# Optimization experiments

Hardware: AMD Instinct MI355X
Metric: run time of the kernel (lower is better)

## Reference

```python
import jax, jax.numpy as jnp
import numpy as np
import math

EPS = 1e-12


def _cmul(ar, ai, br, bi):
    return ar * br - ai * bi, ar * bi + ai * br


def _wilson_seed(x):
    # x: (B, 4, L, L) -> conj of canonical Wilson-line path, (B, L, L) re/im
    ux_r, ux_i, uy_r, uy_i = x[:, 0], x[:, 1], x[:, 2], x[:, 3]
    B, L, _ = ux_r.shape
    dt = x.dtype

    def step(c, u):
        cr, ci = c
        ur, ui = u
        nr, ni = _cmul(cr, ci, ur, ui)
        return (nr, ni), (nr, ni)

    # cumulative complex product along x at y=0
    init_r = jnp.ones((B,), dt)
    init_i = jnp.zeros((B,), dt)
    xs = (ux_r[:, :-1, 0].T, ux_i[:, :-1, 0].T)  # (L-1, B)
    _, (axr, axi) = jax.lax.scan(step, (init_r, init_i), xs)
    x_axis_r = jnp.concatenate([init_r[None], axr], 0).T  # (B, L)
    x_axis_i = jnp.concatenate([init_i[None], axi], 0).T

    # cumulative complex product along y, vectorized over x
    ys = (jnp.moveaxis(uy_r[:, :, :-1], 2, 0), jnp.moveaxis(uy_i[:, :, :-1], 2, 0))  # (L-1, B, L)
    _, (pr, pi_) = jax.lax.scan(step, (x_axis_r, x_axis_i), ys)
    path_r = jnp.moveaxis(jnp.concatenate([x_axis_r[None], pr], 0), 0, 2)  # (B, L, L)
    path_i = jnp.moveaxis(jnp.concatenate([x_axis_i[None], pi_], 0), 0, 2)
    return path_r, -path_i  # conjugate


def _wrap(t):
    return (t + math.pi) % (2.0 * math.pi) - math.pi


def _initial_features(x):
    seed_r, seed_i = _wilson_seed(x)
    ax = jnp.arctan2(x[:, 1], x[:, 0])
    ay = jnp.arctan2(x[:, 3], x[:, 2])
    plaq = _wrap(ax + jnp.roll(ay, -1, axis=1) - jnp.roll(ax, -1, axis=2) - ay)
    pc = jnp.cos(plaq)
    pavg = (pc + jnp.roll(pc, 1, 1) + jnp.roll(pc, -1, 1)
            + jnp.roll(pc, 1, 2) + jnp.roll(pc, -1, 2)) / 5.0
    scalars = jnp.stack([jnp.ones_like(pc), pc, pavg], axis=1)  # (B, 3, L, L)
    return seed_r[:, None] * scalars, seed_i[:, None] * scalars


def _transport_fwd(fr, fi, x, mu):
    lr, li = (x[:, 0], x[:, 1]) if mu == 0 else (x[:, 2], x[:, 3])
    sr = jnp.roll(fr, -1, axis=mu + 2)
    si = jnp.roll(fi, -1, axis=mu + 2)
    return _cmul(lr[:, None], li[:, None], sr, si)


def _transport_bwd(fr, fi, x, mu):
    lr, li = (x[:, 0], x[:, 1]) if mu == 0 else (x[:, 2], x[:, 3])
    cr = jnp.roll(lr, 1, axis=mu + 1)
    ci = jnp.roll(-li, 1, axis=mu + 1)
    sr = jnp.roll(fr, 1, axis=mu + 2)
    si = jnp.roll(fi, 1, axis=mu + 2)
    return _cmul(cr[:, None], ci[:, None], sr, si)


def _lconv(fr, fi, x, center, fwd_w, bwd_w):
    out_r = jnp.einsum('oi,bixy->boxy', center, fr)
    out_i = jnp.einsum('oi,bixy->boxy', center, fi)
    for mu in range(2):
        fr2, fi2 = _transport_fwd(fr, fi, x, mu)
        br2, bi2 = _transport_bwd(fr, fi, x, mu)
        out_r = out_r + jnp.einsum('oi,bixy->boxy', fwd_w[mu], fr2) \
                      + jnp.einsum('oi,bixy->boxy', bwd_w[mu], br2)
        out_i = out_i + jnp.einsum('oi,bixy->boxy', fwd_w[mu], fi2) \
                      + jnp.einsum('oi,bixy->boxy', bwd_w[mu], bi2)
    return out_r, out_i


def _modrelu(fr, fi, bias):
    mag = jnp.sqrt(fr * fr + fi * fi + EPS)
    act = jax.nn.relu(mag + bias[None, :, None, None])
    scale = act / jnp.maximum(mag, EPS)
    return fr * scale, fi * scale


def setup_inputs() -> dict:
    key = jax.random.key(0)
    ks = jax.random.split(key, 11)
    B, L, H, O = 64, 128, 16, 8
    s = 0.1
    return {
        'x': jax.random.normal(ks[0], (B, 4, L, L), jnp.float32),
        'center1': s * jax.random.normal(ks[1], (H, 3), jnp.float32),
        'fwd_w1': s * jax.random.normal(ks[2], (2, H, 3), jnp.float32),
        'bwd_w1': s * jax.random.normal(ks[3], (2, H, 3), jnp.float32),
        'bias1': jnp.zeros((H,), jnp.float32),
        'center2': s * jax.random.normal(ks[4], (O, H), jnp.float32),
        'fwd_w2': s * jax.random.normal(ks[5], (2, O, H), jnp.float32),
        'bwd_w2': s * jax.random.normal(ks[6], (2, O, H), jnp.float32),
        'bias2': jnp.zeros((O,), jnp.float32),
        'ro_weight': s * jax.random.normal(ks[7], (O,), jnp.float32),
        'ro_bias': jnp.zeros((1,), jnp.float32),
    }


def reference(x, center1, fwd_w1, bwd_w1, bias1, center2, fwd_w2, bwd_w2, bias2, ro_weight, ro_bias):
    fr, fi = _initial_features(x)
    fr, fi = _lconv(fr, fi, x, center1, fwd_w1, bwd_w1)
    fr, fi = _modrelu(fr, fi, bias1)
    fr, fi = _lconv(fr, fi, x, center2, fwd_w2, bwd_w2)
    fr, fi = _modrelu(fr, fi, bias2)
    inv = fr * fr + fi * fi
    return jnp.einsum('c,bcxy->bxy', ro_weight, inv)[:, None] + ro_bias.reshape(1, 1, 1, 1)
```

## Files before the change

kernel.cpp:

```cpp
#include <hip/hip_runtime.h>
#include <math.h>

#define LQ   128
#define BQ   64
#define LL   (LQ*LQ)
#define H1   16
#define O2   8
#define TILE 16
#define REG  18
#define NPTS (REG*REG)
#define PCR  22
#define PCN  (PCR*PCR)
#define LKR  23
#define LKN  (LKR*LKR)
#define SDR  20
#define SDN  (SDR*SDR)
#define FSTR 10

typedef float f2 __attribute__((ext_vector_type(2)));
using bf8 = __attribute__((ext_vector_type(8))) short;
using f4  = __attribute__((ext_vector_type(4))) float;

__device__ __forceinline__ int wrapi(int v) { return v & (LQ - 1); }

__device__ __forceinline__ unsigned pack_bf(float hi, float lo) {
    return __builtin_amdgcn_perm(__float_as_uint(hi), __float_as_uint(lo),
                                 0x07060302u);
}

#define WS_W1 ((size_t)BQ * LL)

__global__ __launch_bounds__(256)
void k_scan(const float* __restrict__ x,
            const float* __restrict__ c1, const float* __restrict__ fw1,
            const float* __restrict__ bw1, float* __restrict__ ws) {
    int blk = blockIdx.x;
    if (blk == BQ * 8) {
        int tid = threadIdx.x;
        if (tid < 120) {
            int t = tid / 24, r = tid - t * 24;
            int c = r >> 3, op = r & 7;
            const float* src = (t == 0) ? c1 : (t == 1) ? fw1 : (t == 2) ? bw1
                             : (t == 3) ? (fw1 + 48) : (bw1 + 48);
            float2 v = make_float2(src[(2 * op) * 3 + c], src[(2 * op + 1) * 3 + c]);
            ((float2*)ws)[WS_W1 + tid] = v;
        }
        return;
    }
    int b = blk >> 3, rq = blk & 7;
    int l = threadIdx.x & 63, w = threadIdx.x >> 6;
    const float* x0 = x + (size_t)b * 4 * LL;
    const float* x1 = x0 + LL;

    float ur0 = x0[(2 * l) * LQ],     ui0 = x1[(2 * l) * LQ];
    float ur1 = x0[(2 * l + 1) * LQ], ui1 = x1[(2 * l + 1) * LQ];
    float pr = ur0 * ur1 - ui0 * ui1;
    float pi = ur0 * ui1 + ui0 * ur1;
    for (int d = 1; d < 64; d <<= 1) {
        float qr = __shfl_up(pr, d, 64);
        float qi = __shfl_up(pi, d, 64);
        if (l >= d) {
            float nr = qr * pr - qi * pi;
            float ni = qr * pi + qi * pr;
            pr = nr; pi = ni;
        }
    }
    float er = __shfl_up(pr, 1, 64);
    float ei = __shfl_up(pi, 1, 64);
    if (l == 0) { er = 1.f; ei = 0.f; }
    float e1r = er * ur0 - ei * ui0;
    float e1i = er * ui0 + ei * ur0;

    const float* yrp = x + (size_t)(b * 4 + 2) * LL;
    const float* yip = yrp + LL;
    float4* seed4 = (float4*)ws;

    for (int k = 0; k < 4; ++k) {
        int i = rq * 16 + w * 4 + k;
        float cxr = __shfl((i & 1) ? e1r : er, i >> 1, 64);
        float cxi = __shfl((i & 1) ? e1i : ei, i >> 1, 64);
        const float* yr = yrp + (size_t)i * LQ;
        const float* yi = yip + (size_t)i * LQ;
        float vr0 = yr[2 * l],     vi0 = yi[2 * l];
        float vr1 = yr[2 * l + 1], vi1 = yi[2 * l + 1];
        float sr = vr0 * vr1 - vi0 * vi1;
        float si = vr0 * vi1 + vi0 * vr1;
        for (int d = 1; d < 64; d <<= 1) {
            float qr = __shfl_up(sr, d, 64);
            float qi = __shfl_up(si, d, 64);
            if (l >= d) {
                float nr = qr * sr - qi * si;
                float ni = qr * si + qi * sr;
                sr = nr; si = ni;
            }
        }
        float gr = __shfl_up(sr, 1, 64);
        float gi = __shfl_up(si, 1, 64);
        if (l == 0) { gr = 1.f; gi = 0.f; }
        float s0r = cxr * gr - cxi * gi;
        float s0i = cxr * gi + cxi * gr;
        float s1r = s0r * vr0 - s0i * vi0;
        float s1i = s0r * vi0 + s0i * vr0;
        seed4[((size_t)b * LL + (size_t)i * LQ) / 2 + l] =
            make_float4(s0r, -s0i, s1r, -s1i);
    }
}

__global__ __launch_bounds__(256, 4)
void k_main(const float* __restrict__ x,
            const float* __restrict__ c2, const float* __restrict__ fw2,
            const float* __restrict__ bw2, const float* __restrict__ b1,
            const float* __restrict__ b2,
            const float* __restrict__ ro, const float* __restrict__ rob,
            const float* __restrict__ ws, float* __restrict__ out) {
    __shared__ unsigned s_f1r[NPTS * FSTR];
    __shared__ unsigned s_f1i[NPTS * FSTR];
    __shared__ f2 s_ux[LKN];
    __shared__ f2 s_uy[LKN];
    __shared__ float s_pc[PCN];
    __shared__ f2 s_sd[SDN];
    int tid = threadIdx.x;
    int b = blockIdx.z, i0 = blockIdx.y * TILE, j0 = blockIdx.x * TILE;
    const float* x0 = x + (size_t)b * 4 * LL;
    const float* x1 = x0 + LL;
    const float* x2 = x0 + 2 * LL;
    const float* x3 = x0 + 3 * LL;
    const float2* seed = (const float2*)ws + (size_t)b * LL;
    const float2* W1 = (const float2*)ws + WS_W1;

    bool z1 = true;
#pragma unroll
    for (int h = 0; h < H1; ++h) z1 = z1 && (b1[h] == 0.f);
    bool z2 = true;
#pragma unroll
    for (int o = 0; o < O2; ++o) z2 = z2 && (b2[o] == 0.f);

    for (int p = tid; p < LKN; p += 256) {
        int ri = p / LKR, rj = p - ri * LKR;
        int gi = wrapi(i0 - 3 + ri), gj = wrapi(j0 - 3 + rj);
        int idx = gi * LQ + gj;
        s_ux[p] = (f2){x0[idx], x1[idx]};
        s_uy[p] = (f2){x2[idx], x3[idx]};
    }
    for (int p = tid; p < SDN; p += 256) {
        int ri = p / SDR, rj = p - ri * SDR;
        int gi = wrapi(i0 - 2 + ri), gj = wrapi(j0 - 2 + rj);
        float2 s = seed[gi * LQ + gj];
        s_sd[p] = (f2){s.x, s.y};
    }
    __syncthreads();

    for (int p = tid; p < PCN; p += 256) {
        int ri = p / PCR, rj = p - ri * PCR;
        int lb = ri * LKR + rj;
        f2 u1 = s_ux[lb];
        f2 u2 = s_uy[lb + LKR];
        f2 u3 = s_ux[lb + 1];
        f2 u4 = s_uy[lb];
        float ar = u1.x * u2.x - u1.y * u2.y, ai = u1.x * u2.y + u1.y * u2.x;
        float br = ar * u3.x + ai * u3.y,     bi = -ar * u3.y + ai * u3.x;
        float zr = br * u4.x + bi * u4.y,     zi = -br * u4.y + bi * u4.x;
        s_pc[p] = zr * __frsqrt_rn(fmaf(zr, zr, zi * zi) + 1e-30f);
    }
    __syncthreads();

#pragma unroll
    for (int pass = 0; pass < 2; ++pass) {
        int p = tid + pass * 256;
        if (pass == 1 && p >= NPTS) break;
        int ri = p / REG, rj = p - ri * REG;
        int sc = (ri + 1) * SDR + (rj + 1);
        int lb = (ri + 2) * LKR + (rj + 2);
        int cb = (ri + 2) * PCR + (rj + 2);

        f2 t[5]; float tc[5], tv[5];
        {
            f2 SC = s_sd[sc], SXP = s_sd[sc + SDR], SXM = s_sd[sc - SDR];
            f2 SYP = s_sd[sc + 1], SYM = s_sd[sc - 1];
            f2 lx = s_ux[lb], ly = s_uy[lb];
            f2 mx = s_ux[lb - LKR], my = s_uy[lb - 1];
            t[0] = SC;
            t[1] = (f2){lx.x * SXP.x - lx.y * SXP.y, lx.x * SXP.y + lx.y * SXP.x};
            t[2] = (f2){mx.x * SXM.x + mx.y * SXM.y, mx.x * SXM.y - mx.y * SXM.x};
            t[3] = (f2){ly.x * SYP.x - ly.y * SYP.y, ly.x * SYP.y + ly.y * SYP.x};
            t[4] = (f2){my.x * SYM.x + my.y * SYM.y, my.x * SYM.y - my.y * SYM.x};
            float p00 = s_pc[cb];
            float pP0 = s_pc[cb + PCR],     pM0 = s_pc[cb - PCR];
            float p0P = s_pc[cb + 1],       p0M = s_pc[cb - 1];
            float pP20 = s_pc[cb + 2*PCR],  pM20 = s_pc[cb - 2*PCR];
            float p0P2 = s_pc[cb + 2],      p0M2 = s_pc[cb - 2];
            float pPP = s_pc[cb + PCR + 1], pPM = s_pc[cb + PCR - 1];
            float pMP = s_pc[cb - PCR + 1], pMM = s_pc[cb - PCR - 1];
            tc[0] = p00; tc[1] = pP0; tc[2] = pM0; tc[3] = p0P; tc[4] = p0M;
            tv[0] = (p00 + pP0 + pM0 + p0P + p0M) * 0.2f;
            tv[1] = (pP0 + pP20 + p00 + pPP + pPM) * 0.2f;
            tv[2] = (pM0 + p00 + pM20 + pMP + pMM) * 0.2f;
            tv[3] = (p0P + pPP + pMP + p0P2 + p00) * 0.2f;
            tv[4] = (p0M + pPM + pMM + p00 + p0M2) * 0.2f;
        }

        f2 accr[8], acci[8];
#pragma unroll
        for (int op = 0; op < 8; ++op) { accr[op] = (f2){0.f, 0.f}; acci[op] = (f2){0.f, 0.f}; }
#pragma unroll
        for (int q = 0; q < 5; ++q) {
            f2 tcv = (f2){tc[q], tc[q]}, tvv = (f2){tv[q], tv[q]};
            f2 trv = (f2){t[q].x, t[q].x}, tiv = (f2){t[q].y, t[q].y};
            const float2* Wq = W1 + q * 24;
#pragma unroll
            for (int op = 0; op < 8; ++op) {
                float2 w0 = Wq[op], w1 = Wq[8 + op], w2 = Wq[16 + op];
                f2 mp = (f2){w0.x, w0.y};
                mp += (f2){w1.x, w1.y} * tcv;
                mp += (f2){w2.x, w2.y} * tvv;
                accr[op] += mp * trv;
                acci[op] += mp * tiv;
            }
        }
        if (!z1) {
#pragma unroll
            for (int op = 0; op < 8; ++op) {
                f2 q2 = accr[op] * accr[op] + acci[op] * acci[op] + (f2){1e-12f, 1e-12f};
                float s0 = fmaxf(fmaf(b1[2 * op],     __frsqrt_rn(q2.x), 1.f), 0.f);
                float s1 = fmaxf(fmaf(b1[2 * op + 1], __frsqrt_rn(q2.y), 1.f), 0.f);
                f2 sv = (f2){s0, s1};
                accr[op] *= sv; acci[op] *= sv;
            }
        }
        unsigned* fr_ = &s_f1r[p * FSTR];
        unsigned* fi_ = &s_f1i[p * FSTR];
#pragma unroll
        for (int d = 0; d < 4; ++d) {
            unsigned r0 = pack_bf(accr[2*d].y,   accr[2*d].x);
            unsigned r1 = pack_bf(accr[2*d+1].y, accr[2*d+1].x);
            unsigned q0 = pack_bf(acci[2*d].y,   acci[2*d].x);
            unsigned q1 = pack_bf(acci[2*d+1].y, acci[2*d+1].x);
            *(uint2*)&fr_[2*d] = make_uint2(r0, r1);
            *(uint2*)&fi_[2*d] = make_uint2(q0, q1);
        }
    }
    __syncthreads();

    int lane = tid & 63, w = tid >> 6;
    int quad = lane >> 4, nIdx = lane & 15;
    int half = quad >> 1;
    int koff = (quad & 1) * 4;

    const float* wLo[3] = {c2, bw2, bw2 + O2 * H1};
    const float* wHi[3] = {fw2, fw2 + O2 * H1, (const float*)0};
    bf8 afr[3];
#pragma unroll
    for (int pq = 0; pq < 3; ++pq) {
        bf8 z = {0, 0, 0, 0, 0, 0, 0, 0};
        const float* wsrc = half ? wHi[pq] : wLo[pq];
        int row = half ? (nIdx - 8) : nIdx;
        bool valid = half ? (nIdx >= 8 && wsrc != 0) : (nIdx < 8);
        if (valid) {
            const float* wp = wsrc + row * H1 + (quad & 1) * 8;
            float4 wa = *(const float4*)wp;
            float4 wb = *(const float4*)(wp + 4);
            uint4 u;
            u.x = pack_bf(wa.y, wa.x);
            u.y = pack_bf(wa.w, wa.z);
            u.z = pack_bf(wb.y, wb.x);
            u.w = pack_bf(wb.w, wb.z);
            __builtin_memcpy(&z, &u, 16);
        }
        afr[pq] = z;
    }
    float4 ro_lo = *(const float4*)ro;
    float4 ro_hi = *(const float4*)(ro + 4);
    float4 b2_lo = *(const float4*)b2;
    float4 b2_hi = *(const float4*)(b2 + 4);
    float4 zf4 = make_float4(0.f, 0.f, 0.f, 0.f);
    float4 rv = (quad == 0) ? ro_lo : ((quad == 1) ? ro_hi : zf4);
    float4 bv = (quad == 0) ? b2_lo : ((quad == 1) ? b2_hi : zf4);
    float rob0 = rob[0];

    for (int g = 0; g < 4; ++g) {
        int row = w * 4 + g;
        int posc = (row + 1) * REG + (nIdx + 1);
        int lb2 = (row + 3) * LKR + (nIdx + 3);
        f2 lx = s_ux[lb2], ly = s_uy[lb2];
        f2 mx = s_ux[lb2 - LKR], my = s_uy[lb2 - 1];

        float Lr[3], Li[3];
        Lr[0] = half ? lx.x : 1.f;   Li[0] = half ? lx.y : 0.f;
        Lr[1] = half ? ly.x : mx.x;  Li[1] = half ? ly.y : -mx.y;
        Lr[2] = half ? 0.f : my.x;   Li[2] = half ? 0.f : -my.y;
        int dpl[3];
        dpl[0] = half ? REG : 0;
        dpl[1] = half ? 1 : -REG;
        dpl[2] = -1;

        f4 a2r = {0.f, 0.f, 0.f, 0.f}, a2i = {0.f, 0.f, 0.f, 0.f};
#pragma unroll
        for (int pq = 0; pq < 3; ++pq) {
            int base = (posc + dpl[pq]) * FSTR + koff;
            uint2 rlo = *(const uint2*)&s_f1r[base];
            uint2 rhi = *(const uint2*)&s_f1r[base + 2];
            uint2 ilo = *(const uint2*)&s_f1i[base];
            uint2 ihi = *(const uint2*)&s_f1i[base + 2];
            bf8 br, bi;
            uint4 ur = {rlo.x, rlo.y, rhi.x, rhi.y};
            uint4 ui = {ilo.x, ilo.y, ihi.x, ihi.y};
            __builtin_memcpy(&br, &ur, 16);
            __builtin_memcpy(&bi, &ui, 16);
            f4 zc = {0.f, 0.f, 0.f, 0.f};
            f4 sr = __builtin_amdgcn_mfma_f32_16x16x32_bf16(afr[pq], br, zc, 0, 0, 0);
            f4 si = __builtin_amdgcn_mfma_f32_16x16x32_bf16(afr[pq], bi, zc, 0, 0, 0);
            a2r += Lr[pq] * sr - Li[pq] * si;
            a2i += Lr[pq] * si + Li[pq] * sr;
        }

#pragma unroll
        for (int c = 0; c < 4; ++c) {
            a2r[c] += __shfl_xor(a2r[c], 32, 64);
            a2i[c] += __shfl_xor(a2i[c], 32, 64);
        }

        f4 q4 = a2r * a2r + a2i * a2i;
        float res;
        if (z2) {
            res = rv.x * q4.x + rv.y * q4.y + rv.z * q4.z + rv.w * q4.w;
        } else {
            float bvv[4] = {bv.x, bv.y, bv.z, bv.w};
            float rvv[4] = {rv.x, rv.y, rv.z, rv.w};
            res = 0.f;
#pragma unroll
            for (int r = 0; r < 4; ++r) {
                float qq = q4[r];
                float s = fmaxf(fmaf(bvv[r], __frsqrt_rn(qq + 1e-12f), 1.f), 0.f);
                res = fmaf(rvv[r], s * s * qq, res);
            }
        }
        res += __shfl_xor(res, 16, 64);
        if (quad == 0)
            out[(size_t)b * LL + (size_t)(i0 + row) * LQ + (j0 + nIdx)] = res + rob0;
    }
}

extern "C" void kernel_launch(void* const* d_in, const int* in_sizes, int n_in,
                              void* d_out, int out_size, void* d_ws, size_t ws_size,
                              hipStream_t stream) {
    const float* x   = (const float*)d_in[0];
    const float* c1  = (const float*)d_in[1];
    const float* fw1 = (const float*)d_in[2];
    const float* bw1 = (const float*)d_in[3];
    const float* b1  = (const float*)d_in[4];
    const float* c2  = (const float*)d_in[5];
    const float* fw2 = (const float*)d_in[6];
    const float* bw2 = (const float*)d_in[7];
    const float* b2  = (const float*)d_in[8];
    const float* ro  = (const float*)d_in[9];
    const float* rob = (const float*)d_in[10];
    float* out = (float*)d_out;
    float* ws  = (float*)d_ws;

    k_scan<<<BQ * 8 + 1, 256, 0, stream>>>(x, c1, fw1, bw1, ws);
    dim3 grid(LQ / TILE, LQ / TILE, BQ);
    k_main<<<grid, 256, 0, stream>>>(x, c2, fw2, bw2, b1, b2,
                                     ro, rob, ws, out);
}
```

Baseline: 135.3 us.

## Compute first lattice conv layer with bf16 MFMA and swizzled shared layout

Layer 1 of the lattice convolution was scalar FMA over 5 transports x 3 scalars x 16 channels. It now builds a 15-wide bf16 feature vector per point, transposes it across lanes with shuffles, and multiplies by the layer-1 weight matrix with 16x16x32 bf16 MFMA. The seed staging buffer in shared memory is dropped in favour of direct global reads. Layer-1 output moves to a single rotated/swizzled 16-word-per-point LDS layout so layer 2 can use 128-bit loads, and occupancy is raised to 5 blocks per CU. Costs include extra shuffles and lower precision in layer 1, since inputs are rounded to bf16 before the multiply.

```diff
diff --git a/kernel.cpp b/kernel.cpp
--- a/kernel.cpp
+++ b/kernel.cpp
@@ -13,9 +13,6 @@
 #define PCN  (PCR*PCR)
 #define LKR  23
 #define LKN  (LKR*LKR)
-#define SDR  20
-#define SDN  (SDR*SDR)
-#define FSTR 10
 
 typedef float f2 __attribute__((ext_vector_type(2)));
 using bf8 = __attribute__((ext_vector_type(8))) short;
@@ -26,6 +23,11 @@
 __device__ __forceinline__ unsigned pack_bf(float hi, float lo) {
     return __builtin_amdgcn_perm(__float_as_uint(hi), __float_as_uint(lo),
                                  0x07060302u);
+}
+__device__ __forceinline__ unsigned cvt_pk_bf16(float lo, float hi) {
+    unsigned r;
+    asm("v_cvt_pk_bf16_f32 %0, %1, %2" : "=v"(r) : "v"(lo), "v"(hi));
+    return r;
 }
 
 #define WS_W1 ((size_t)BQ * LL)
@@ -106,19 +108,17 @@
     }
 }
 
-__global__ __launch_bounds__(256, 4)
+__global__ __launch_bounds__(256, 5)
 void k_main(const float* __restrict__ x,
             const float* __restrict__ c2, const float* __restrict__ fw2,
             const float* __restrict__ bw2, const float* __restrict__ b1,
             const float* __restrict__ b2,
             const float* __restrict__ ro, const float* __restrict__ rob,
             const float* __restrict__ ws, float* __restrict__ out) {
-    __shared__ unsigned s_f1r[NPTS * FSTR];
-    __shared__ unsigned s_f1i[NPTS * FSTR];
+    __shared__ __align__(16) unsigned s_f1[NPTS * 16];
     __shared__ f2 s_ux[LKN];
     __shared__ f2 s_uy[LKN];
     __shared__ float s_pc[PCN];
-    __shared__ f2 s_sd[SDN];
     int tid = threadIdx.x;
     int b = blockIdx.z, i0 = blockIdx.y * TILE, j0 = blockIdx.x * TILE;
     const float* x0 = x + (size_t)b * 4 * LL;
@@ -128,12 +128,34 @@
     const float2* seed = (const float2*)ws + (size_t)b * LL;
     const float2* W1 = (const float2*)ws + WS_W1;
 
+    int lane = tid & 63, w = tid >> 6;
+    int kc = lane >> 4, h = lane & 15, half = kc >> 1;
+
     bool z1 = true;
 #pragma unroll
-    for (int h = 0; h < H1; ++h) z1 = z1 && (b1[h] == 0.f);
+    for (int hh = 0; hh < H1; ++hh) z1 = z1 && (b1[hh] == 0.f);
     bool z2 = true;
 #pragma unroll
-    for (int o = 0; o < O2; ++o) z2 = z2 && (b2[o] == 0.f);
+    for (int oo = 0; oo < O2; ++oo) z2 = z2 && (b2[oo] == 0.f);
+
+    bf8 a1 = {0, 0, 0, 0, 0, 0, 0, 0};
+    if (kc < 2) {
+        float v[8];
+#pragma unroll
+        for (int j = 0; j < 8; ++j) {
+            int k = kc * 8 + j;
+            float val = 0.f;
+            if (k < 15) {
+                int q = k / 3, c = k - q * 3;
+                val = ((const float*)(W1 + (q * 24 + c * 8 + (h >> 1))))[h & 1];
+            }
+            v[j] = val;
+        }
+        unsigned dw[4];
+#pragma unroll
+        for (int d = 0; d < 4; ++d) dw[d] = cvt_pk_bf16(v[2 * d], v[2 * d + 1]);
+        __builtin_memcpy(&a1, dw, 16);
+    }
 
     for (int p = tid; p < LKN; p += 256) {
         int ri = p / LKR, rj = p - ri * LKR;
@@ -141,12 +163,6 @@
         int idx = gi * LQ + gj;
         s_ux[p] = (f2){x0[idx], x1[idx]};
         s_uy[p] = (f2){x2[idx], x3[idx]};
-    }
-    for (int p = tid; p < SDN; p += 256) {
-        int ri = p / SDR, rj = p - ri * SDR;
-        int gi = wrapi(i0 - 2 + ri), gj = wrapi(j0 - 2 + rj);
-        float2 s = seed[gi * LQ + gj];
-        s_sd[p] = (f2){s.x, s.y};
     }
     __syncthreads();
 
@@ -164,87 +180,105 @@
     }
     __syncthreads();
 
-#pragma unroll
-    for (int pass = 0; pass < 2; ++pass) {
-        int p = tid + pass * 256;
-        if (pass == 1 && p >= NPTS) break;
-        int ri = p / REG, rj = p - ri * REG;
-        int sc = (ri + 1) * SDR + (rj + 1);
+    for (int wp = w * 64; wp < NPTS; wp += 256) {
+        int p = wp + lane;
+        int pp = (p < NPTS) ? p : (NPTS - 1);
+        int ri = pp / REG, rj = pp - ri * REG;
         int lb = (ri + 2) * LKR + (rj + 2);
         int cb = (ri + 2) * PCR + (rj + 2);
 
-        f2 t[5]; float tc[5], tv[5];
+        int gi0 = wrapi(i0 - 1 + ri), gim = wrapi(i0 - 2 + ri), gip = wrapi(i0 + ri);
+        int gj0 = wrapi(j0 - 1 + rj), gjm = wrapi(j0 - 2 + rj), gjp = wrapi(j0 + rj);
+        float2 SC  = seed[gi0 * LQ + gj0];
+        float2 SXP = seed[gip * LQ + gj0];
+        float2 SXM = seed[gim * LQ + gj0];
+        float2 SYP = seed[gi0 * LQ + gjp];
+        float2 SYM = seed[gi0 * LQ + gjm];
+
+        f2 lx = s_ux[lb], ly = s_uy[lb];
+        f2 mx = s_ux[lb - LKR], my = s_uy[lb - 1];
+        float tr[5], ti[5], tc[5], tv[5];
+        tr[0] = SC.x;                          ti[0] = SC.y;
+        tr[1] = lx.x * SXP.x - lx.y * SXP.y;   ti[1] = lx.x * SXP.y + lx.y * SXP.x;
+        tr[2] = mx.x * SXM.x + mx.y * SXM.y;   ti[2] = mx.x * SXM.y - mx.y * SXM.x;
+        tr[3] = ly.x * SYP.x - ly.y * SYP.y;   ti[3] = ly.x * SYP.y + ly.y * SYP.x;
+        tr[4] = my.x * SYM.x + my.y * SYM.y;   ti[4] = my.x * SYM.y - my.y * SYM.x;
+
+        float p00 = s_pc[cb];
+        float pP0 = s_pc[cb + PCR],     pM0 = s_pc[cb - PCR];
+        float p0P = s_pc[cb + 1],       p0M = s_pc[cb - 1];
+        float pP20 = s_pc[cb + 2*PCR],  pM20 = s_pc[cb - 2*PCR];
+        float p0P2 = s_pc[cb + 2],      p0M2 = s_pc[cb - 2];
+        float pPP = s_pc[cb + PCR + 1], pPM = s_pc[cb + PCR - 1];
+        float pMP = s_pc[cb - PCR + 1], pMM = s_pc[cb - PCR - 1];
+        tc[0] = p00; tc[1] = pP0; tc[2] = pM0; tc[3] = p0P; tc[4] = p0M;
+        tv[0] = (p00 + pP0 + pM0 + p0P + p0M) * 0.2f;
+        tv[1] = (pP0 + pP20 + p00 + pPP + pPM) * 0.2f;
+        tv[2] = (pM0 + p00 + pM20 + pMP + pMM) * 0.2f;
+        tv[3] = (p0P + pPP + pMP + p0P2 + p00) * 0.2f;
+        tv[4] = (p0M + pPM + pMM + p00 + p0M2) * 0.2f;
+
+        unsigned fr8[8], fi8[8];
         {
-            f2 SC = s_sd[sc], SXP = s_sd[sc + SDR], SXM = s_sd[sc - SDR];
-            f2 SYP = s_sd[sc + 1], SYM = s_sd[sc - 1];
-            f2 lx = s_ux[lb], ly = s_uy[lb];
-            f2 mx = s_ux[lb - LKR], my = s_uy[lb - 1];
-            t[0] = SC;
-            t[1] = (f2){lx.x * SXP.x - lx.y * SXP.y, lx.x * SXP.y + lx.y * SXP.x};
-            t[2] = (f2){mx.x * SXM.x + mx.y * SXM.y, mx.x * SXM.y - mx.y * SXM.x};
-            t[3] = (f2){ly.x * SYP.x - ly.y * SYP.y, ly.x * SYP.y + ly.y * SYP.x};
-            t[4] = (f2){my.x * SYM.x + my.y * SYM.y, my.x * SYM.y - my.y * SYM.x};
-            float p00 = s_pc[cb];
-            float pP0 = s_pc[cb + PCR],     pM0 = s_pc[cb - PCR];
-            float p0P = s_pc[cb + 1],       p0M = s_pc[cb - 1];
-            float pP20 = s_pc[cb + 2*PCR],  pM20 = s_pc[cb - 2*PCR];
-            float p0P2 = s_pc[cb + 2],      p0M2 = s_pc[cb - 2];
-            float pPP = s_pc[cb + PCR + 1], pPM = s_pc[cb + PCR - 1];
-            float pMP = s_pc[cb - PCR + 1], pMM = s_pc[cb - PCR - 1];
-            tc[0] = p00; tc[1] = pP0; tc[2] = pM0; tc[3] = p0P; tc[4] = p0M;
-            tv[0] = (p00 + pP0 + pM0 + p0P + p0M) * 0.2f;
-            tv[1] = (pP0 + pP20 + p00 + pPP + pPM) * 0.2f;
-            tv[2] = (pM0 + p00 + pM20 + pMP + pMM) * 0.2f;
-            tv[3] = (p0P + pPP + pMP + p0P2 + p00) * 0.2f;
-            tv[4] = (p0M + pPM + pMM + p00 + p0M2) * 0.2f;
-        }
-
-        f2 accr[8], acci[8];
-#pragma unroll
-        for (int op = 0; op < 8; ++op) { accr[op] = (f2){0.f, 0.f}; acci[op] = (f2){0.f, 0.f}; }
-#pragma unroll
-        for (int q = 0; q < 5; ++q) {
-            f2 tcv = (f2){tc[q], tc[q]}, tvv = (f2){tv[q], tv[q]};
-            f2 trv = (f2){t[q].x, t[q].x}, tiv = (f2){t[q].y, t[q].y};
-            const float2* Wq = W1 + q * 24;
-#pragma unroll
-            for (int op = 0; op < 8; ++op) {
-                float2 w0 = Wq[op], w1 = Wq[8 + op], w2 = Wq[16 + op];
-                f2 mp = (f2){w0.x, w0.y};
-                mp += (f2){w1.x, w1.y} * tcv;
-                mp += (f2){w2.x, w2.y} * tvv;
-                accr[op] += mp * trv;
-                acci[op] += mp * tiv;
-            }
-        }
-        if (!z1) {
-#pragma unroll
-            for (int op = 0; op < 8; ++op) {
-                f2 q2 = accr[op] * accr[op] + acci[op] * acci[op] + (f2){1e-12f, 1e-12f};
-                float s0 = fmaxf(fmaf(b1[2 * op],     __frsqrt_rn(q2.x), 1.f), 0.f);
-                float s1 = fmaxf(fmaf(b1[2 * op + 1], __frsqrt_rn(q2.y), 1.f), 0.f);
-                f2 sv = (f2){s0, s1};
-                accr[op] *= sv; acci[op] *= sv;
-            }
-        }
-        unsigned* fr_ = &s_f1r[p * FSTR];
-        unsigned* fi_ = &s_f1i[p * FSTR];
-#pragma unroll
-        for (int d = 0; d < 4; ++d) {
-            unsigned r0 = pack_bf(accr[2*d].y,   accr[2*d].x);
-            unsigned r1 = pack_bf(accr[2*d+1].y, accr[2*d+1].x);
-            unsigned q0 = pack_bf(acci[2*d].y,   acci[2*d].x);
-            unsigned q1 = pack_bf(acci[2*d+1].y, acci[2*d+1].x);
-            *(uint2*)&fr_[2*d] = make_uint2(r0, r1);
-            *(uint2*)&fi_[2*d] = make_uint2(q0, q1);
+            float Fr[16], Fi[16];
+#pragma unroll
+            for (int q = 0; q < 5; ++q) {
+                Fr[3*q]   = tr[q];         Fi[3*q]   = ti[q];
+                Fr[3*q+1] = tc[q]*tr[q];   Fi[3*q+1] = tc[q]*ti[q];
+                Fr[3*q+2] = tv[q]*tr[q];   Fi[3*q+2] = tv[q]*ti[q];
+            }
+            Fr[15] = 0.f; Fi[15] = 0.f;
+#pragma unroll
+            for (int d = 0; d < 8; ++d) {
+                fr8[d] = cvt_pk_bf16(Fr[2*d], Fr[2*d+1]);
+                fi8[d] = cvt_pk_bf16(Fi[2*d], Fi[2*d+1]);
+            }
+        }
+
+        int ng = (NPTS - wp + 15) >> 4;
+        if (ng > 4) ng = 4;
+        for (int g = 0; g < ng; ++g) {
+            int src = g * 16 + h;
+            unsigned brw[4], biw[4];
+#pragma unroll
+            for (int d = 0; d < 4; ++d) {
+                unsigned rlo = __shfl(fr8[d],     src, 64);
+                unsigned rhi = __shfl(fr8[d + 4], src, 64);
+                unsigned ilo = __shfl(fi8[d],     src, 64);
+                unsigned ihi = __shfl(fi8[d + 4], src, 64);
+                brw[d] = (kc == 0) ? rlo : ((kc == 1) ? rhi : 0u);
+                biw[d] = (kc == 0) ? ilo : ((kc == 1) ? ihi : 0u);
+            }
+            bf8 br, bi;
+            __builtin_memcpy(&br, brw, 16);
+            __builtin_memcpy(&bi, biw, 16);
+            f4 zc = {0.f, 0.f, 0.f, 0.f};
+            f4 Dr = __builtin_amdgcn_mfma_f32_16x16x32_bf16(a1, br, zc, 0, 0, 0);
+            f4 Di = __builtin_amdgcn_mfma_f32_16x16x32_bf16(a1, bi, zc, 0, 0, 0);
+            int P = wp + g * 16 + h;
+            if (P < NPTS) {
+                if (!z1) {
+#pragma unroll
+                    for (int r = 0; r < 4; ++r) {
+                        float q2 = Dr[r]*Dr[r] + Di[r]*Di[r] + 1e-12f;
+                        float s = fmaxf(fmaf(b1[4*kc + r], __frsqrt_rn(q2), 1.f), 0.f);
+                        Dr[r] *= s; Di[r] *= s;
+                    }
+                }
+                unsigned pr0 = cvt_pk_bf16(Dr[0], Dr[1]);
+                unsigned pr1 = cvt_pk_bf16(Dr[2], Dr[3]);
+                unsigned pi0 = cvt_pk_bf16(Di[0], Di[1]);
+                unsigned pi1 = cvt_pk_bf16(Di[2], Di[3]);
+                int rot = (P >> 1) & 3;
+                int base = P * 16 + ((kc & 1) << 1);
+                int ar = base + ((((kc >> 1) + rot) & 3) << 2);
+                int ai = base + ((((kc >> 1) + 2 + rot) & 3) << 2);
+                *(uint2*)&s_f1[ar] = make_uint2(pr0, pr1);
+                *(uint2*)&s_f1[ai] = make_uint2(pi0, pi1);
+            }
         }
     }
     __syncthreads();
-
-    int lane = tid & 63, w = tid >> 6;
-    int quad = lane >> 4, nIdx = lane & 15;
-    int half = quad >> 1;
-    int koff = (quad & 1) * 4;
 
     const float* wLo[3] = {c2, bw2, bw2 + O2 * H1};
     const float* wHi[3] = {fw2, fw2 + O2 * H1, (const float*)0};
@@ -253,12 +287,12 @@
     for (int pq = 0; pq < 3; ++pq) {
         bf8 z = {0, 0, 0, 0, 0, 0, 0, 0};
         const float* wsrc = half ? wHi[pq] : wLo[pq];
-        int row = half ? (nIdx - 8) : nIdx;
-        bool valid = half ? (nIdx >= 8 && wsrc != 0) : (nIdx < 8);
+        int wrow = half ? (h - 8) : h;
+        bool valid = half ? (h >= 8 && wsrc != 0) : (h < 8);
         if (valid) {
-            const float* wp = wsrc + row * H1 + (quad & 1) * 8;
-            float4 wa = *(const float4*)wp;
-            float4 wb = *(const float4*)(wp + 4);
+            const float* wp2 = wsrc + wrow * H1 + (kc & 1) * 8;
+            float4 wa = *(const float4*)wp2;
+            float4 wb = *(const float4*)(wp2 + 4);
             uint4 u;
             u.x = pack_bf(wa.y, wa.x);
             u.y = pack_bf(wa.w, wa.z);
@@ -273,14 +307,14 @@
     float4 b2_lo = *(const float4*)b2;
     float4 b2_hi = *(const float4*)(b2 + 4);
     float4 zf4 = make_float4(0.f, 0.f, 0.f, 0.f);
-    float4 rv = (quad == 0) ? ro_lo : ((quad == 1) ? ro_hi : zf4);
-    float4 bv = (quad == 0) ? b2_lo : ((quad == 1) ? b2_hi : zf4);
+    float4 rv = (kc == 0) ? ro_lo : ((kc == 1) ? ro_hi : zf4);
+    float4 bv = (kc == 0) ? b2_lo : ((kc == 1) ? b2_hi : zf4);
     float rob0 = rob[0];
 
     for (int g = 0; g < 4; ++g) {
         int row = w * 4 + g;
-        int posc = (row + 1) * REG + (nIdx + 1);
-        int lb2 = (row + 3) * LKR + (nIdx + 3);
+        int posc = (row + 1) * REG + (h + 1);
+        int lb2 = (row + 3) * LKR + (h + 3);
         f2 lx = s_ux[lb2], ly = s_uy[lb2];
         f2 mx = s_ux[lb2 - LKR], my = s_uy[lb2 - 1];
 
@@ -296,14 +330,12 @@
         f4 a2r = {0.f, 0.f, 0.f, 0.f}, a2i = {0.f, 0.f, 0.f, 0.f};
 #pragma unroll
         for (int pq = 0; pq < 3; ++pq) {
-            int base = (posc + dpl[pq]) * FSTR + koff;
-            uint2 rlo = *(const uint2*)&s_f1r[base];
-            uint2 rhi = *(const uint2*)&s_f1r[base + 2];
-            uint2 ilo = *(const uint2*)&s_f1i[base];
-            uint2 ihi = *(const uint2*)&s_f1i[base + 2];
+            int posc2 = posc + dpl[pq];
+            int rot2 = (posc2 >> 1) & 3;
+            int bb = posc2 * 16;
+            uint4 ur = *(const uint4*)&s_f1[bb + ((((kc & 1) + rot2) & 3) << 2)];
+            uint4 ui = *(const uint4*)&s_f1[bb + ((((kc & 1) + 2 + rot2) & 3) << 2)];
             bf8 br, bi;
-            uint4 ur = {rlo.x, rlo.y, rhi.x, rhi.y};
-            uint4 ui = {ilo.x, ilo.y, ihi.x, ihi.y};
             __builtin_memcpy(&br, &ur, 16);
             __builtin_memcpy(&bi, &ui, 16);
             f4 zc = {0.f, 0.f, 0.f, 0.f};
@@ -335,8 +367,8 @@
             }
         }
         res += __shfl_xor(res, 16, 64);
-        if (quad == 0)
-            out[(size_t)b * LL + (size_t)(i0 + row) * LQ + (j0 + nIdx)] = res + rob0;
+        if (kc == 0)
+            out[(size_t)b * LL + (size_t)(i0 + row) * LQ + (j0 + h)] = res + rob0;
     }
 }
 
```

Measured after the change: 133.5 us. Within noise of the previous version (-1.3%).
